# Performance work log

Measured on AMD Instinct MI355X. Metric: run time of the kernel, lower is better.

Reference implementation:

```python
import jax, jax.numpy as jnp
import numpy as np

S, B, E, H = 2048, 2, 1024, 16
DH = E // H
SCALING = DH ** -0.5


def setup_inputs() -> dict:
    key = jax.random.key(0)
    ks = jax.random.split(key, 9)
    std = 1.0 / np.sqrt(E)
    return {
        "query": jax.random.normal(ks[0], (S, B, E), jnp.float32),
        "wq": jax.random.normal(ks[1], (E, E), jnp.float32) * std,
        "bq": jax.random.normal(ks[2], (E,), jnp.float32) * 0.02,
        "wk": jax.random.normal(ks[3], (E, E), jnp.float32) * std,
        "bk": jax.random.normal(ks[4], (E,), jnp.float32) * 0.02,
        "wv": jax.random.normal(ks[5], (E, E), jnp.float32) * std,
        "bv": jax.random.normal(ks[6], (E,), jnp.float32) * 0.02,
        "wo": jax.random.normal(ks[7], (E, E), jnp.float32) * std,
        "bo": jax.random.normal(ks[8], (E,), jnp.float32) * 0.02,
    }


def reference(query, wq, bq, wk, bk, wv, bv, wo, bo):
    # query: [S, B, E] (time, batch, channel), self-attention: key=value=query
    q = (query @ wq.T + bq) * SCALING          # fairseq scales q, not scores
    k = query @ wk.T + bk
    v = query @ wv.T + bv
    # split heads: [S, B, H, DH]
    q = q.reshape(S, B, H, DH)
    k = k.reshape(S, B, H, DH)
    v = v.reshape(S, B, H, DH)
    scores = jnp.einsum("qbhd,kbhd->bhqk", q, k)   # [B, H, S, S]
    probs = jax.nn.softmax(scores, axis=-1)
    ctx = jnp.einsum("bhqk,kbhd->qbhd", probs, v)  # [S, B, H, DH]
    ctx = ctx.reshape(S, B, E)
    return ctx @ wo.T + bo                          # [S, B, E]
```

## Files before the change

### kernel.cpp

```cpp
#include <hip/hip_runtime.h>
#include <hip/hip_bf16.h>
#include <stdint.h>

#define S_LEN 2048
#define BATCH 2
#define EMB   1024
#define NH    16
#define DHEAD 64
#define ROWS  (S_LEN*BATCH)
#define SCALE_Q 0.18033688011112042f
#define DEFER_THR 11.0f

typedef __attribute__((ext_vector_type(8))) short bf16x8;
typedef __attribute__((ext_vector_type(4))) float f32x4;

typedef const __attribute__((address_space(1))) void* gas_ptr;
typedef __attribute__((address_space(3))) void* las_ptr;
#define GLD16(g, l) __builtin_amdgcn_global_load_lds((gas_ptr)(g), (las_ptr)(l), 16, 0, 0)

__device__ __forceinline__ unsigned short f2b(float f) {
  union { float f; unsigned int u; } v; v.f = f;
  unsigned int u = v.u;
  unsigned int r = (u + 0x7FFFu + ((u >> 16) & 1u)) >> 16;
  return (unsigned short)r;
}

__device__ __forceinline__ unsigned cvt_pk_bf16(float lo, float hi) {
  unsigned r;
  asm("v_cvt_pk_bf16_f32 %0, %1, %2" : "=v"(r) : "v"(lo), "v"(hi));
  return r;
}

__device__ __forceinline__ void cvt8(const float* __restrict__ s,
                                     unsigned short* __restrict__ d, size_t i) {
  float4 a = *reinterpret_cast<const float4*>(s + i);
  float4 b = *reinterpret_cast<const float4*>(s + i + 4);
  uint4 o;
  o.x = (unsigned)f2b(a.x) | ((unsigned)f2b(a.y) << 16);
  o.y = (unsigned)f2b(a.z) | ((unsigned)f2b(a.w) << 16);
  o.z = (unsigned)f2b(b.x) | ((unsigned)f2b(b.y) << 16);
  o.w = (unsigned)f2b(b.z) | ((unsigned)f2b(b.w) << 16);
  *reinterpret_cast<uint4*>(d + i) = o;
}

__global__ __launch_bounds__(256) void cvt_kernel(const float* __restrict__ s,
                                                  unsigned short* __restrict__ d) {
  size_t i = ((size_t)blockIdx.x * 256 + threadIdx.x) * 8;
  cvt8(s, d, i);
}

__global__ __launch_bounds__(256) void cvt4_kernel(
    const float* __restrict__ s0, const float* __restrict__ s1,
    const float* __restrict__ s2, const float* __restrict__ s3,
    unsigned short* __restrict__ d0, unsigned short* __restrict__ d1,
    unsigned short* __restrict__ d2, unsigned short* __restrict__ d3) {
  const float* s; unsigned short* d;
  switch (blockIdx.y) {
    case 0:  s = s0; d = d0; break;
    case 1:  s = s1; d = d1; break;
    case 2:  s = s2; d = d2; break;
    default: s = s3; d = d3; break;
  }
  size_t i = ((size_t)blockIdx.x * 256 + threadIdx.x) * 8;
  cvt8(s, d, i);
}

__device__ __forceinline__ void gemm_mainloop(const unsigned short* __restrict__ A,
                                              const unsigned short* __restrict__ Bw,
                                              int m0, int n0, f32x4 acc[4][4]) {
  __shared__ unsigned short Ab[128 * 64];
  __shared__ unsigned short Bb[128 * 64];
  const int t    = threadIdx.x;
  const int lane = t & 63;
  const int w    = t >> 6;
  const int wr   = w >> 1, wc = w & 1;
  const int lm   = lane & 15;
  const int lq   = lane >> 4;

  f32x4 zf = {0.0f, 0.0f, 0.0f, 0.0f};
#pragma unroll
  for (int i = 0; i < 4; ++i)
#pragma unroll
    for (int j = 0; j < 4; ++j) acc[i][j] = zf;

  for (int k0 = 0; k0 < EMB; k0 += 64) {
#pragma unroll
    for (int q = 0; q < 4; ++q) {
      int c = t + q * 256;
      int r = c >> 3, ci = c & 7;
      int lc = ci ^ (r & 7);
      GLD16(A  + (size_t)(m0 + r) * EMB + k0 + lc * 8,
            (char*)&Ab[0] + (size_t)(q * 256 + w * 64) * 16);
      GLD16(Bw + (size_t)(n0 + r) * EMB + k0 + lc * 8,
            (char*)&Bb[0] + (size_t)(q * 256 + w * 64) * 16);
    }
    asm volatile("s_waitcnt vmcnt(0)" ::: "memory");
    __syncthreads();

#pragma unroll
    for (int kk = 0; kk < 2; ++kk) {
      bf16x8 af[4], bfr[4];
#pragma unroll
      for (int i = 0; i < 4; ++i) {
        int ra = wr * 64 + i * 16 + lm;
        af[i] = *reinterpret_cast<const bf16x8*>(
            &Ab[ra * 64 + ((kk * 4 + lq) ^ (ra & 7)) * 8]);
      }
#pragma unroll
      for (int j = 0; j < 4; ++j) {
        int rb = wc * 64 + j * 16 + lm;
        bfr[j] = *reinterpret_cast<const bf16x8*>(
            &Bb[rb * 64 + ((kk * 4 + lq) ^ (rb & 7)) * 8]);
      }
#pragma unroll
      for (int i = 0; i < 4; ++i)
#pragma unroll
        for (int j = 0; j < 4; ++j)
          acc[i][j] = __builtin_amdgcn_mfma_f32_16x16x32_bf16(af[i], bfr[j], acc[i][j], 0, 0, 0);
    }
    __syncthreads();
  }
}

__global__ __launch_bounds__(256) void gemm_qkv_kernel(
    const unsigned short* __restrict__ X,
    const unsigned short* __restrict__ Wq, const unsigned short* __restrict__ Wk,
    const unsigned short* __restrict__ Wv,
    const float* __restrict__ bq, const float* __restrict__ bk, const float* __restrict__ bv,
    unsigned short* __restrict__ Qb, unsigned short* __restrict__ Kb,
    unsigned short* __restrict__ Vb) {
  const int m0 = blockIdx.x * 128;
  const int n0 = blockIdx.y * 128;
  const int z  = blockIdx.z;
  const unsigned short* Bw = (z == 0) ? Wq : (z == 1) ? Wk : Wv;
  const float* bias        = (z == 0) ? bq : (z == 1) ? bk : bv;
  unsigned short* Out      = (z == 0) ? Qb : (z == 1) ? Kb : Vb;
  const float scale        = (z == 0) ? SCALE_Q : 1.0f;

  f32x4 acc[4][4];
  gemm_mainloop(X, Bw, m0, n0, acc);

  const int lane = threadIdx.x & 63;
  const int w    = threadIdx.x >> 6;
  const int wr   = w >> 1, wc = w & 1;
  const int lm   = lane & 15, lq = lane >> 4;
#pragma unroll
  for (int j = 0; j < 4; ++j) {
    int col = n0 + wc * 64 + j * 16 + lm;
    int h = col >> 6, dd = col & 63;
    float bc = bias[col];
#pragma unroll
    for (int i = 0; i < 4; ++i) {
#pragma unroll
      for (int r = 0; r < 4; ++r) {
        int row = m0 + wr * 64 + i * 16 + lq * 4 + r;
        int s = row >> 1, b = row & 1;
        float v = (acc[i][j][r] + bc) * scale;
        Out[((size_t)(b * NH + h) * S_LEN + s) * DHEAD + dd] = f2b(v);
      }
    }
  }
}

__global__ __launch_bounds__(256) void gemm_out_kernel(
    const unsigned short* __restrict__ Ctx, const unsigned short* __restrict__ Wo,
    const float* __restrict__ bo, float* __restrict__ Out) {
  const int m0 = blockIdx.x * 128;
  const int n0 = blockIdx.y * 128;
  f32x4 acc[4][4];
  gemm_mainloop(Ctx, Wo, m0, n0, acc);

  const int lane = threadIdx.x & 63;
  const int w    = threadIdx.x >> 6;
  const int wr   = w >> 1, wc = w & 1;
  const int lm   = lane & 15, lq = lane >> 4;
#pragma unroll
  for (int j = 0; j < 4; ++j) {
    int col = n0 + wc * 64 + j * 16 + lm;
    float bc = bo[col];
#pragma unroll
    for (int i = 0; i < 4; ++i) {
#pragma unroll
      for (int r = 0; r < 4; ++r) {
        int row = m0 + wr * 64 + i * 16 + lq * 4 + r;
        Out[(size_t)row * EMB + col] = acc[i][j][r] + bc;
      }
    }
  }
}

__global__ __launch_bounds__(256) void transpose_v_kernel(
    const unsigned short* __restrict__ Vb, unsigned short* __restrict__ Vtg) {
  const int bh = blockIdx.x;
  const int kb = blockIdx.y * 64;
  const unsigned short* src = Vb + (size_t)bh * S_LEN * DHEAD;
  unsigned short* dst = Vtg + (size_t)bh * DHEAD * S_LEN;
  __shared__ unsigned short T[64][80];
  const int t = threadIdx.x;
#pragma unroll
  for (int q = 0; q < 2; ++q) {
    int c = t + q * 256;
    int r = c >> 3, j = (c & 7) * 8;
    bf16x8 v = *reinterpret_cast<const bf16x8*>(src + (size_t)(kb + r) * DHEAD + j);
    *reinterpret_cast<bf16x8*>(&T[r][j]) = v;
  }
  __syncthreads();
  int d = t >> 2, kvc = (t & 3) * 16;
  bf16x8 o0, o1;
#pragma unroll
  for (int e = 0; e < 8; ++e) o0[e] = (short)T[kvc + e][d];
#pragma unroll
  for (int e = 0; e < 8; ++e) o1[e] = (short)T[kvc + 8 + e][d];
  *reinterpret_cast<bf16x8*>(dst + (size_t)d * S_LEN + kb + kvc) = o0;
  *reinterpret_cast<bf16x8*>(dst + (size_t)d * S_LEN + kb + kvc + 8) = o1;
}

__global__ __launch_bounds__(512) void attn_kernel(
    const unsigned short* __restrict__ Qb, const unsigned short* __restrict__ Kb,
    const unsigned short* __restrict__ Vtg, unsigned short* __restrict__ Ctx) {
  const int bh = blockIdx.x;
  const int q0 = blockIdx.y * 128;
  const int t    = threadIdx.x;
  const int lane = t & 63;
  const int w    = t >> 6;
  const int lm   = lane & 15, lq = lane >> 4;
  const unsigned short* Q  = Qb  + (size_t)bh * S_LEN * DHEAD;
  const unsigned short* K  = Kb  + (size_t)bh * S_LEN * DHEAD;
  const unsigned short* Vt = Vtg + (size_t)bh * DHEAD * S_LEN;

  __shared__ unsigned short Kl[2][64 * 64];
  __shared__ unsigned short Vl[2][64 * 64];
  __shared__ unsigned short Pl[8][16 * 72];

  const int qw = q0 + w * 16;

  bf16x8 aq[2];
#pragma unroll
  for (int c = 0; c < 2; ++c)
    aq[c] = *reinterpret_cast<const bf16x8*>(
        Q + (size_t)(qw + lm) * DHEAD + c * 32 + lq * 8);

  f32x4 zf = {0.0f, 0.0f, 0.0f, 0.0f};
  f32x4 accO[4];
#pragma unroll
  for (int ni = 0; ni < 4; ++ni) accO[ni] = zf;
  float m_s = -1e30f, l_s = 0.0f;

  auto STAGE = [&](int b, int kb) {
    int r = t >> 3, p = t & 7;
    int lc = p ^ (r & 7);
    GLD16(K  + (size_t)(kb + r) * DHEAD + lc * 8,
          (char*)&Kl[b][0] + (size_t)(w * 64) * 16);
    GLD16(Vt + (size_t)r * S_LEN + kb + lc * 8,
          (char*)&Vl[b][0] + (size_t)(w * 64) * 16);
  };

  const int NT = S_LEN / 64;
  STAGE(0, 0);
  STAGE(1, 64);

  for (int it = 0; it < NT; ++it) {
    const int cur = it & 1;
    if (it < NT - 1) {
      asm volatile("s_waitcnt vmcnt(2)" ::: "memory");
    } else {
      asm volatile("s_waitcnt vmcnt(0)" ::: "memory");
    }
    __builtin_amdgcn_s_barrier();

    f32x4 p4[4];
    __builtin_amdgcn_s_setprio(1);
#pragma unroll
    for (int ji = 0; ji < 4; ++ji) {
      int rr = ji * 16 + lm;
      bf16x8 k0 = *reinterpret_cast<const bf16x8*>(
          &Kl[cur][rr * 64 + ((lq) ^ (rr & 7)) * 8]);
      bf16x8 k1 = *reinterpret_cast<const bf16x8*>(
          &Kl[cur][rr * 64 + ((4 + lq) ^ (rr & 7)) * 8]);
      f32x4 s0 = __builtin_amdgcn_mfma_f32_16x16x32_bf16(k0, aq[0], zf, 0, 0, 0);
      p4[ji]   = __builtin_amdgcn_mfma_f32_16x16x32_bf16(k1, aq[1], s0, 0, 0, 0);
    }
    __builtin_amdgcn_s_setprio(0);

    float t0 = fmaxf(fmaxf(p4[0][0], p4[0][1]), fmaxf(p4[0][2], p4[0][3]));
    float t1 = fmaxf(fmaxf(p4[1][0], p4[1][1]), fmaxf(p4[1][2], p4[1][3]));
    float t2 = fmaxf(fmaxf(p4[2][0], p4[2][1]), fmaxf(p4[2][2], p4[2][3]));
    float t3 = fmaxf(fmaxf(p4[3][0], p4[3][1]), fmaxf(p4[3][2], p4[3][3]));
    float tm = fmaxf(fmaxf(t0, t1), fmaxf(t2, t3));
    tm = fmaxf(tm, __shfl_xor(tm, 16));
    tm = fmaxf(tm, __shfl_xor(tm, 32));

    if (!__all(tm - m_s <= DEFER_THR)) {
      float mn = fmaxf(m_s, tm);
      float sc = exp2f(m_s - mn);
      l_s *= sc;
      m_s = mn;
#pragma unroll
      for (int r = 0; r < 4; ++r) {
        float scr = __shfl(sc, lq * 4 + r);
#pragma unroll
        for (int ni = 0; ni < 4; ++ni) accO[ni][r] *= scr;
      }
    }

    float ps = 0.0f;
#pragma unroll
    for (int ji = 0; ji < 4; ++ji)
#pragma unroll
      for (int r = 0; r < 4; ++r) {
        float e = exp2f(p4[ji][r] - m_s);
        p4[ji][r] = e;
        ps += e;
      }
    ps += __shfl_xor(ps, 16);
    ps += __shfl_xor(ps, 32);
    l_s += ps;

    unsigned short* Pw = &Pl[w][0];
#pragma unroll
    for (int ji = 0; ji < 4; ++ji) {
      uint2 u;
      u.x = cvt_pk_bf16(p4[ji][0], p4[ji][1]);
      u.y = cvt_pk_bf16(p4[ji][2], p4[ji][3]);
      *reinterpret_cast<uint2*>(&Pw[lm * 72 + ji * 16 + lq * 4]) = u;
    }

    bf16x8 ap[2];
#pragma unroll
    for (int c = 0; c < 2; ++c)
      ap[c] = *reinterpret_cast<const bf16x8*>(&Pw[lm * 72 + c * 32 + lq * 8]);
    __builtin_amdgcn_s_setprio(1);
#pragma unroll
    for (int ni = 0; ni < 4; ++ni) {
      int dd = ni * 16 + lm;
#pragma unroll
      for (int c = 0; c < 2; ++c) {
        bf16x8 bv = *reinterpret_cast<const bf16x8*>(
            &Vl[cur][dd * 64 + ((c * 4 + lq) ^ (dd & 7)) * 8]);
        accO[ni] = __builtin_amdgcn_mfma_f32_16x16x32_bf16(ap[c], bv, accO[ni], 0, 0, 0);
      }
    }
    __builtin_amdgcn_s_setprio(0);

    asm volatile("s_waitcnt lgkmcnt(0)" ::: "memory");
    __builtin_amdgcn_sched_barrier(0);
    __builtin_amdgcn_s_barrier();

    if (it + 2 < NT) STAGE(cur, (it + 2) * 64);
  }

  const int b = bh >> 4, h = bh & 15;
#pragma unroll
  for (int r = 0; r < 4; ++r) {
    float rl = 1.0f / __shfl(l_s, lq * 4 + r);
    int srow = qw + lq * 4 + r;
    size_t rowbase = ((size_t)srow * BATCH + b) * EMB + (size_t)h * 64;
#pragma unroll
    for (int ni = 0; ni < 4; ++ni)
      Ctx[rowbase + ni * 16 + lm] = f2b(accO[ni][r] * rl);
  }
}

extern "C" void kernel_launch(void* const* d_in, const int* in_sizes, int n_in,
                              void* d_out, int out_size, void* d_ws, size_t ws_size,
                              hipStream_t stream) {
  const float* query = (const float*)d_in[0];
  const float* wq = (const float*)d_in[1];
  const float* bq = (const float*)d_in[2];
  const float* wk = (const float*)d_in[3];
  const float* bk = (const float*)d_in[4];
  const float* wv = (const float*)d_in[5];
  const float* bv = (const float*)d_in[6];
  const float* wo = (const float*)d_in[7];
  const float* bo = (const float*)d_in[8];
  float* out = (float*)d_out;

  unsigned short* p = (unsigned short*)d_ws;
  unsigned short* Xbf = p;                        p += (size_t)ROWS * EMB;
  unsigned short* Wqb = p;                        p += (size_t)EMB * EMB;
  unsigned short* Wkb = p;                        p += (size_t)EMB * EMB;
  unsigned short* Wvb = p;                        p += (size_t)EMB * EMB;
  unsigned short* Wob = p;                        p += (size_t)EMB * EMB;
  unsigned short* Qb  = p;                        p += (size_t)ROWS * EMB;
  unsigned short* Kb  = p;                        p += (size_t)ROWS * EMB;
  unsigned short* Vb  = p;                        p += (size_t)ROWS * EMB;
  unsigned short* Ctx = p;                        p += (size_t)ROWS * EMB;
  unsigned short* Vtg = Xbf;

  cvt_kernel<<<ROWS * EMB / 8 / 256, 256, 0, stream>>>(query, Xbf);
  cvt4_kernel<<<dim3(EMB * EMB / 8 / 256, 4), 256, 0, stream>>>(
      wq, wk, wv, wo, Wqb, Wkb, Wvb, Wob);
  gemm_qkv_kernel<<<dim3(ROWS / 128, EMB / 128, 3), 256, 0, stream>>>(
      Xbf, Wqb, Wkb, Wvb, bq, bk, bv, Qb, Kb, Vb);
  transpose_v_kernel<<<dim3(BATCH * NH, S_LEN / 64), 256, 0, stream>>>(Vb, Vtg);
  attn_kernel<<<dim3(BATCH * NH, S_LEN / 128), 512, 0, stream>>>(Qb, Kb, Vtg, Ctx);
  gemm_out_kernel<<<dim3(ROWS / 128, EMB / 128), 256, 0, stream>>>(Ctx, Wob, bo, out);
}
```

Measured before the change: 222.4 us.

## Fuse V transpose into QKV GEMM, merge conversions, use raw exp, precompute LDS offsets

The V projection epilogue now stages its tile through shared memory and writes V already transposed, which removes the separate transpose kernel and its global round trip. The two fp32-to-bf16 conversion kernels are merged into one launch. The attention kernel precomputes swizzled LDS byte offsets for K and V outside the loop. It also replaces exp2f with the raw v_exp_f32 instruction, which may change precision handling for denormal inputs.

```diff
diff --git a/kernel.cpp b/kernel.cpp
--- a/kernel.cpp
+++ b/kernel.cpp
@@ -28,6 +28,12 @@
 __device__ __forceinline__ unsigned cvt_pk_bf16(float lo, float hi) {
   unsigned r;
   asm("v_cvt_pk_bf16_f32 %0, %1, %2" : "=v"(r) : "v"(lo), "v"(hi));
+  return r;
+}
+
+__device__ __forceinline__ float exp2_raw(float x) {
+  float r;
+  asm("v_exp_f32 %0, %1" : "=v"(r) : "v"(x));
   return r;
 }
 
@@ -43,33 +49,33 @@
   *reinterpret_cast<uint4*>(d + i) = o;
 }
 
-__global__ __launch_bounds__(256) void cvt_kernel(const float* __restrict__ s,
-                                                  unsigned short* __restrict__ d) {
-  size_t i = ((size_t)blockIdx.x * 256 + threadIdx.x) * 8;
-  cvt8(s, d, i);
-}
-
-__global__ __launch_bounds__(256) void cvt4_kernel(
-    const float* __restrict__ s0, const float* __restrict__ s1,
-    const float* __restrict__ s2, const float* __restrict__ s3,
-    unsigned short* __restrict__ d0, unsigned short* __restrict__ d1,
-    unsigned short* __restrict__ d2, unsigned short* __restrict__ d3) {
-  const float* s; unsigned short* d;
-  switch (blockIdx.y) {
-    case 0:  s = s0; d = d0; break;
-    case 1:  s = s1; d = d1; break;
-    case 2:  s = s2; d = d2; break;
-    default: s = s3; d = d3; break;
-  }
-  size_t i = ((size_t)blockIdx.x * 256 + threadIdx.x) * 8;
-  cvt8(s, d, i);
+__global__ __launch_bounds__(256) void cvt_all_kernel(
+    const float* __restrict__ query,
+    const float* __restrict__ wq, const float* __restrict__ wk,
+    const float* __restrict__ wv, const float* __restrict__ wo,
+    unsigned short* __restrict__ Xbf,
+    unsigned short* __restrict__ Wqb, unsigned short* __restrict__ Wkb,
+    unsigned short* __restrict__ Wvb, unsigned short* __restrict__ Wob) {
+  int id = blockIdx.x;
+  const float* s; unsigned short* d; size_t off;
+  if (id < 2048) { s = query; d = Xbf; off = (size_t)id * 2048; }
+  else {
+    int wsel = (id - 2048) >> 9;
+    off = (size_t)((id - 2048) & 511) * 2048;
+    switch (wsel) {
+      case 0:  s = wq; d = Wqb; break;
+      case 1:  s = wk; d = Wkb; break;
+      case 2:  s = wv; d = Wvb; break;
+      default: s = wo; d = Wob; break;
+    }
+  }
+  cvt8(s, d, off + (size_t)threadIdx.x * 8);
 }
 
 __device__ __forceinline__ void gemm_mainloop(const unsigned short* __restrict__ A,
                                               const unsigned short* __restrict__ Bw,
-                                              int m0, int n0, f32x4 acc[4][4]) {
-  __shared__ unsigned short Ab[128 * 64];
-  __shared__ unsigned short Bb[128 * 64];
+                                              int m0, int n0, f32x4 acc[4][4],
+                                              unsigned short* Ab, unsigned short* Bb) {
   const int t    = threadIdx.x;
   const int lane = t & 63;
   const int w    = t >> 6;
@@ -90,9 +96,9 @@
       int r = c >> 3, ci = c & 7;
       int lc = ci ^ (r & 7);
       GLD16(A  + (size_t)(m0 + r) * EMB + k0 + lc * 8,
-            (char*)&Ab[0] + (size_t)(q * 256 + w * 64) * 16);
+            (char*)Ab + (size_t)(q * 256 + w * 64) * 16);
       GLD16(Bw + (size_t)(n0 + r) * EMB + k0 + lc * 8,
-            (char*)&Bb[0] + (size_t)(q * 256 + w * 64) * 16);
+            (char*)Bb + (size_t)(q * 256 + w * 64) * 16);
     }
     asm volatile("s_waitcnt vmcnt(0)" ::: "memory");
     __syncthreads();
@@ -128,17 +134,83 @@
     const unsigned short* __restrict__ Wv,
     const float* __restrict__ bq, const float* __restrict__ bk, const float* __restrict__ bv,
     unsigned short* __restrict__ Qb, unsigned short* __restrict__ Kb,
-    unsigned short* __restrict__ Vb) {
+    unsigned short* __restrict__ Vtg) {
+  __shared__ unsigned short SH[2][128 * 64];
   const int m0 = blockIdx.x * 128;
   const int n0 = blockIdx.y * 128;
   const int z  = blockIdx.z;
   const unsigned short* Bw = (z == 0) ? Wq : (z == 1) ? Wk : Wv;
   const float* bias        = (z == 0) ? bq : (z == 1) ? bk : bv;
-  unsigned short* Out      = (z == 0) ? Qb : (z == 1) ? Kb : Vb;
-  const float scale        = (z == 0) ? SCALE_Q : 1.0f;
 
   f32x4 acc[4][4];
-  gemm_mainloop(X, Bw, m0, n0, acc);
+  gemm_mainloop(X, Bw, m0, n0, acc, SH[0], SH[1]);
+
+  const int t    = threadIdx.x;
+  const int lane = t & 63;
+  const int w    = t >> 6;
+  const int wr   = w >> 1, wc = w & 1;
+  const int lm   = lane & 15, lq = lane >> 4;
+
+  if (z != 2) {
+    unsigned short* Out = (z == 0) ? Qb : Kb;
+    const float scale   = (z == 0) ? SCALE_Q : 1.0f;
+#pragma unroll
+    for (int j = 0; j < 4; ++j) {
+      int col = n0 + wc * 64 + j * 16 + lm;
+      int h = col >> 6, dd = col & 63;
+      float bc = bias[col];
+#pragma unroll
+      for (int i = 0; i < 4; ++i) {
+#pragma unroll
+        for (int r = 0; r < 4; ++r) {
+          int row = m0 + wr * 64 + i * 16 + lq * 4 + r;
+          int s = row >> 1, b = row & 1;
+          float v = (acc[i][j][r] + bc) * scale;
+          Out[((size_t)(b * NH + h) * S_LEN + s) * DHEAD + dd] = f2b(v);
+        }
+      }
+    }
+  } else {
+    unsigned short* T = &SH[0][0];
+#pragma unroll
+    for (int j = 0; j < 4; ++j) {
+      int col = wc * 64 + j * 16 + lm;
+      float bc = bias[n0 + col];
+#pragma unroll
+      for (int i = 0; i < 4; ++i) {
+#pragma unroll
+        for (int r = 0; r < 4; ++r) {
+          int row = wr * 64 + i * 16 + lq * 4 + r;
+          int idx = (row & 1) * 64 + (row >> 1);
+          int chunk = idx >> 3, within = idx & 7;
+          int pchunk = (chunk & 8) | ((chunk ^ col) & 7);
+          T[col * 128 + pchunk * 8 + within] = f2b(acc[i][j][r] + bc);
+        }
+      }
+    }
+    __syncthreads();
+#pragma unroll
+    for (int itr = 0; itr < 8; ++itr) {
+      int u = (t >> 3) + itr * 32;
+      int col = u & 127, b = u >> 7;
+      int c3 = t & 7;
+      int pchunk = (b * 8) | ((c3 ^ col) & 7);
+      bf16x8 vv = *reinterpret_cast<const bf16x8*>(&T[col * 128 + pchunk * 8]);
+      int h = (n0 + col) >> 6, dd = (n0 + col) & 63;
+      *reinterpret_cast<bf16x8*>(
+          Vtg + ((size_t)(b * NH + h) * DHEAD + dd) * S_LEN + (m0 >> 1) + c3 * 8) = vv;
+    }
+  }
+}
+
+__global__ __launch_bounds__(256) void gemm_out_kernel(
+    const unsigned short* __restrict__ Ctx, const unsigned short* __restrict__ Wo,
+    const float* __restrict__ bo, float* __restrict__ Out) {
+  __shared__ unsigned short SH[2][128 * 64];
+  const int m0 = blockIdx.x * 128;
+  const int n0 = blockIdx.y * 128;
+  f32x4 acc[4][4];
+  gemm_mainloop(Ctx, Wo, m0, n0, acc, SH[0], SH[1]);
 
   const int lane = threadIdx.x & 63;
   const int w    = threadIdx.x >> 6;
@@ -147,36 +219,6 @@
 #pragma unroll
   for (int j = 0; j < 4; ++j) {
     int col = n0 + wc * 64 + j * 16 + lm;
-    int h = col >> 6, dd = col & 63;
-    float bc = bias[col];
-#pragma unroll
-    for (int i = 0; i < 4; ++i) {
-#pragma unroll
-      for (int r = 0; r < 4; ++r) {
-        int row = m0 + wr * 64 + i * 16 + lq * 4 + r;
-        int s = row >> 1, b = row & 1;
-        float v = (acc[i][j][r] + bc) * scale;
-        Out[((size_t)(b * NH + h) * S_LEN + s) * DHEAD + dd] = f2b(v);
-      }
-    }
-  }
-}
-
-__global__ __launch_bounds__(256) void gemm_out_kernel(
-    const unsigned short* __restrict__ Ctx, const unsigned short* __restrict__ Wo,
-    const float* __restrict__ bo, float* __restrict__ Out) {
-  const int m0 = blockIdx.x * 128;
-  const int n0 = blockIdx.y * 128;
-  f32x4 acc[4][4];
-  gemm_mainloop(Ctx, Wo, m0, n0, acc);
-
-  const int lane = threadIdx.x & 63;
-  const int w    = threadIdx.x >> 6;
-  const int wr   = w >> 1, wc = w & 1;
-  const int lm   = lane & 15, lq = lane >> 4;
-#pragma unroll
-  for (int j = 0; j < 4; ++j) {
-    int col = n0 + wc * 64 + j * 16 + lm;
     float bc = bo[col];
 #pragma unroll
     for (int i = 0; i < 4; ++i) {
@@ -187,32 +229,6 @@
       }
     }
   }
-}
-
-__global__ __launch_bounds__(256) void transpose_v_kernel(
-    const unsigned short* __restrict__ Vb, unsigned short* __restrict__ Vtg) {
-  const int bh = blockIdx.x;
-  const int kb = blockIdx.y * 64;
-  const unsigned short* src = Vb + (size_t)bh * S_LEN * DHEAD;
-  unsigned short* dst = Vtg + (size_t)bh * DHEAD * S_LEN;
-  __shared__ unsigned short T[64][80];
-  const int t = threadIdx.x;
-#pragma unroll
-  for (int q = 0; q < 2; ++q) {
-    int c = t + q * 256;
-    int r = c >> 3, j = (c & 7) * 8;
-    bf16x8 v = *reinterpret_cast<const bf16x8*>(src + (size_t)(kb + r) * DHEAD + j);
-    *reinterpret_cast<bf16x8*>(&T[r][j]) = v;
-  }
-  __syncthreads();
-  int d = t >> 2, kvc = (t & 3) * 16;
-  bf16x8 o0, o1;
-#pragma unroll
-  for (int e = 0; e < 8; ++e) o0[e] = (short)T[kvc + e][d];
-#pragma unroll
-  for (int e = 0; e < 8; ++e) o1[e] = (short)T[kvc + 8 + e][d];
-  *reinterpret_cast<bf16x8*>(dst + (size_t)d * S_LEN + kb + kvc) = o0;
-  *reinterpret_cast<bf16x8*>(dst + (size_t)d * S_LEN + kb + kvc + 8) = o1;
 }
 
 __global__ __launch_bounds__(512) void attn_kernel(
@@ -240,6 +256,20 @@
     aq[c] = *reinterpret_cast<const bf16x8*>(
         Q + (size_t)(qw + lm) * DHEAD + c * 32 + lq * 8);
 
+  int koff[2][4], voff[4][2];
+#pragma unroll
+  for (int ji = 0; ji < 4; ++ji) {
+    int rr = ji * 16 + lm;
+    koff[0][ji] = (rr * 64 + ((lq) ^ (rr & 7)) * 8) * 2;
+    koff[1][ji] = (rr * 64 + ((4 + lq) ^ (rr & 7)) * 8) * 2;
+  }
+#pragma unroll
+  for (int ni = 0; ni < 4; ++ni) {
+    int dd = ni * 16 + lm;
+    voff[ni][0] = (dd * 64 + ((lq) ^ (dd & 7)) * 8) * 2;
+    voff[ni][1] = (dd * 64 + ((4 + lq) ^ (dd & 7)) * 8) * 2;
+  }
+
   f32x4 zf = {0.0f, 0.0f, 0.0f, 0.0f};
   f32x4 accO[4];
 #pragma unroll
@@ -268,15 +298,13 @@
     }
     __builtin_amdgcn_s_barrier();
 
+    const char* Kb8 = (const char*)&Kl[cur][0];
     f32x4 p4[4];
     __builtin_amdgcn_s_setprio(1);
 #pragma unroll
     for (int ji = 0; ji < 4; ++ji) {
-      int rr = ji * 16 + lm;
-      bf16x8 k0 = *reinterpret_cast<const bf16x8*>(
-          &Kl[cur][rr * 64 + ((lq) ^ (rr & 7)) * 8]);
-      bf16x8 k1 = *reinterpret_cast<const bf16x8*>(
-          &Kl[cur][rr * 64 + ((4 + lq) ^ (rr & 7)) * 8]);
+      bf16x8 k0 = *reinterpret_cast<const bf16x8*>(Kb8 + koff[0][ji]);
+      bf16x8 k1 = *reinterpret_cast<const bf16x8*>(Kb8 + koff[1][ji]);
       f32x4 s0 = __builtin_amdgcn_mfma_f32_16x16x32_bf16(k0, aq[0], zf, 0, 0, 0);
       p4[ji]   = __builtin_amdgcn_mfma_f32_16x16x32_bf16(k1, aq[1], s0, 0, 0, 0);
     }
@@ -292,7 +320,7 @@
 
     if (!__all(tm - m_s <= DEFER_THR)) {
       float mn = fmaxf(m_s, tm);
-      float sc = exp2f(m_s - mn);
+      float sc = exp2_raw(m_s - mn);
       l_s *= sc;
       m_s = mn;
 #pragma unroll
@@ -308,7 +336,7 @@
     for (int ji = 0; ji < 4; ++ji)
 #pragma unroll
       for (int r = 0; r < 4; ++r) {
-        float e = exp2f(p4[ji][r] - m_s);
+        float e = exp2_raw(p4[ji][r] - m_s);
         p4[ji][r] = e;
         ps += e;
       }
@@ -329,14 +357,13 @@
 #pragma unroll
     for (int c = 0; c < 2; ++c)
       ap[c] = *reinterpret_cast<const bf16x8*>(&Pw[lm * 72 + c * 32 + lq * 8]);
+    const char* Vb8 = (const char*)&Vl[cur][0];
     __builtin_amdgcn_s_setprio(1);
 #pragma unroll
     for (int ni = 0; ni < 4; ++ni) {
-      int dd = ni * 16 + lm;
 #pragma unroll
       for (int c = 0; c < 2; ++c) {
-        bf16x8 bv = *reinterpret_cast<const bf16x8*>(
-            &Vl[cur][dd * 64 + ((c * 4 + lq) ^ (dd & 7)) * 8]);
+        bf16x8 bv = *reinterpret_cast<const bf16x8*>(Vb8 + voff[ni][c]);
         accO[ni] = __builtin_amdgcn_mfma_f32_16x16x32_bf16(ap[c], bv, accO[ni], 0, 0, 0);
       }
     }
@@ -383,16 +410,13 @@
   unsigned short* Wob = p;                        p += (size_t)EMB * EMB;
   unsigned short* Qb  = p;                        p += (size_t)ROWS * EMB;
   unsigned short* Kb  = p;                        p += (size_t)ROWS * EMB;
-  unsigned short* Vb  = p;                        p += (size_t)ROWS * EMB;
+  unsigned short* Vtg = p;                        p += (size_t)ROWS * EMB;
   unsigned short* Ctx = p;                        p += (size_t)ROWS * EMB;
-  unsigned short* Vtg = Xbf;
-
-  cvt_kernel<<<ROWS * EMB / 8 / 256, 256, 0, stream>>>(query, Xbf);
-  cvt4_kernel<<<dim3(EMB * EMB / 8 / 256, 4), 256, 0, stream>>>(
-      wq, wk, wv, wo, Wqb, Wkb, Wvb, Wob);
+
+  cvt_all_kernel<<<4096, 256, 0, stream>>>(query, wq, wk, wv, wo,
+                                           Xbf, Wqb, Wkb, Wvb, Wob);
   gemm_qkv_kernel<<<dim3(ROWS / 128, EMB / 128, 3), 256, 0, stream>>>(
-      Xbf, Wqb, Wkb, Wvb, bq, bk, bv, Qb, Kb, Vb);
-  transpose_v_kernel<<<dim3(BATCH * NH, S_LEN / 64), 256, 0, stream>>>(Vb, Vtg);
+      Xbf, Wqb, Wkb, Wvb, bq, bk, bv, Qb, Kb, Vtg);
   attn_kernel<<<dim3(BATCH * NH, S_LEN / 128), 512, 0, stream>>>(Qb, Kb, Vtg, Ctx);
   gemm_out_kernel<<<dim3(ROWS / 128, EMB / 128), 256, 0, stream>>>(Ctx, Wob, bo, out);
 }
```

After: 206.7 us. -7.0%, faster.
